# Optimization experiments

Measured on AMD Instinct MI355X. Metric: run time of the kernel, lower is better.

The kernel has to match this reference:

```python
import jax, jax.numpy as jnp
import numpy as np

B, T, N, H = 256, 128, 512, 128  # batch, timesteps, input_size (driving series), hidden


def setup_inputs() -> dict:
    key = jax.random.key(0)
    ks = jax.random.split(key, 7)
    p = lambda k, shape: (jax.random.normal(k, shape, dtype=jnp.float32) * 0.05)
    return {
        "X": jax.random.normal(ks[0], (B, T, N), dtype=jnp.float32),
        # attention linear: in_features = 2H + T, out_features = 1 (stored as a vector + scalar bias)
        "attn_w": p(ks[1], (2 * H + T,)),
        "attn_b": p(ks[2], ()),
        # LSTM cell params, PyTorch layout/gate order (i, f, g, o)
        "w_ih": p(ks[3], (4 * H, N)),
        "w_hh": p(ks[4], (4 * H, H)),
        "b_ih": p(ks[5], (4 * H,)),
        "b_hh": p(ks[6], (4 * H,)),
    }


def reference(X, attn_w, attn_b, w_ih, w_hh, b_ih, b_hh):
    Bn, Tn, Nn = X.shape
    Hh = w_hh.shape[1]
    # split the single attention weight row into the h / s / X-row pieces of the concat
    w_h, w_s, w_x = attn_w[:Hh], attn_w[Hh:2 * Hh], attn_w[2 * Hh:]
    Xp = jnp.swapaxes(X, 1, 2)            # [B, N, T]  (X.permute(0,2,1))
    x_score = Xp @ w_x                    # [B, N], time-invariant part of attention logits

    def step(carry, x_t):                 # x_t: [B, N] = X[:, t, :]
        h, c = carry
        # logits[b,i] = w_h.h[b] + w_s.c[b] + w_x.Xp[b,i] + b  (== Linear on the concat)
        score = x_score + (h @ w_h + c @ w_s + attn_b)[:, None]   # [B, N]
        alpha = jax.nn.softmax(score, axis=1)
        x_tilde = alpha * x_t                                      # [B, N]
        gates = x_tilde @ w_ih.T + h @ w_hh.T + b_ih + b_hh        # [B, 4H]
        i, f, g, o = jnp.split(gates, 4, axis=1)
        c_new = jax.nn.sigmoid(f) * c + jax.nn.sigmoid(i) * jnp.tanh(g)
        h_new = jax.nn.sigmoid(o) * jnp.tanh(c_new)
        return (h_new, c_new), (x_tilde, h_new)

    h0 = jnp.zeros((Bn, Hh), X.dtype)
    (_, _), (Xt, Xe) = jax.lax.scan(step, (h0, h0), jnp.swapaxes(X, 0, 1))
    # scan stacks along time -> [T, B, .]; return [B, T, .]
    return jnp.swapaxes(Xt, 0, 1), jnp.swapaxes(Xe, 0, 1)
```

## Files before the change

kernel.cpp:

```cpp
#include <hip/hip_runtime.h>
#include <hip/hip_bf16.h>

#define Bb 256
#define Tt 128
#define Nn 512
#define Hh 128

typedef __attribute__((ext_vector_type(4))) float floatx4;
typedef __attribute__((ext_vector_type(8))) short short8;
typedef _Float16 h2v_t __attribute__((ext_vector_type(2)));

__device__ __forceinline__ unsigned short f2bf(float f) {
  unsigned u = __float_as_uint(f);
  u += 0x7fffu + ((u >> 16) & 1u);
  return (unsigned short)(u >> 16);
}

__device__ __forceinline__ float sigmoid_fast(float x) {
  return __builtin_amdgcn_rcpf(1.f + __expf(-x));
}
__device__ __forceinline__ float tanh_fast(float x) {
  float e = __expf(2.f * x);
  return 1.f - 2.f * __builtin_amdgcn_rcpf(e + 1.f);
}

__device__ __forceinline__ void lds_barrier() {
  asm volatile("s_waitcnt lgkmcnt(0)" ::: "memory");
  __builtin_amdgcn_s_barrier();
  asm volatile("" ::: "memory");
}

__device__ __forceinline__ void async_load16(const void* g, void* lds) {
  __builtin_amdgcn_global_load_lds(
      (const __attribute__((address_space(1))) unsigned int*)g,
      (__attribute__((address_space(3))) unsigned int*)lds, 16, 0, 0);
}

#if __has_builtin(__builtin_amdgcn_fdot2)
#define FDOT2(a, b, c) __builtin_amdgcn_fdot2((a), (b), (c), false)
#else
__device__ __forceinline__ float fdot2_sw(h2v_t a, h2v_t b, float c) {
  return fmaf((float)a.x, (float)b.x, fmaf((float)a.y, (float)b.y, (c)));
}
#define FDOT2(a, b, c) fdot2_sw((a), (b), (c))
#endif

#define ROT1 0x121
#define ROT4 0x124
template <int CTRL>
__device__ __forceinline__ int rot_i(int x) {
#if __has_builtin(__builtin_amdgcn_update_dpp)
  return __builtin_amdgcn_update_dpp(0, x, CTRL, 0xf, 0xf, true);
#else
  return __shfl(x, (threadIdx.x & ~15) + (((threadIdx.x & 15) + (CTRL & 15)) & 15), 64);
#endif
}
template <int CTRL>
__device__ __forceinline__ float rot_f(float x) {
  return __uint_as_float((unsigned)rot_i<CTRL>((int)__float_as_uint(x)));
}

__global__ void prep_kernel(const float* __restrict__ w_ih,
                            const float* __restrict__ b_ih,
                            const float* __restrict__ b_hh,
                            unsigned short* __restrict__ wb,
                            float* __restrict__ bias) {
  int i = blockIdx.x * 256 + threadIdx.x;
  if (i < 4 * Hh * Nn) wb[i] = f2bf(w_ih[i]);
  if (i < 4 * Hh) bias[i] = b_ih[i] + b_hh[i];
}

__global__ __launch_bounds__(512) void alpha_kernel(const float* __restrict__ X,
                                                    const float* __restrict__ attn_w,
                                                    float* __restrict__ alpha) {
  int b = blockIdx.x;
  int tid = threadIdx.x;
  int c = tid & 127;
  int tp = tid >> 7;
  const float4* Xb = (const float4*)(X + (size_t)b * Tt * Nn) + c;
  const float* wx = attn_w + 2 * Hh;

  float4 acc = {0.f, 0.f, 0.f, 0.f};
#pragma unroll 8
  for (int tt = 0; tt < 32; ++tt) {
    int t = tp * 32 + tt;
    float4 x = Xb[(size_t)t * 128];
    float w = wx[t];
    acc.x = fmaf(x.x, w, acc.x);
    acc.y = fmaf(x.y, w, acc.y);
    acc.z = fmaf(x.z, w, acc.z);
    acc.w = fmaf(x.w, w, acc.w);
  }

  __shared__ float4 s4[512];
  __shared__ float sred[128];
  s4[tid] = acc;
  __syncthreads();

  float4 sc = {0.f, 0.f, 0.f, 0.f};
  if (tid < 128) {
    float4 a = s4[tid], b2 = s4[tid + 128], c2 = s4[tid + 256], d = s4[tid + 384];
    sc.x = a.x + b2.x + c2.x + d.x;
    sc.y = a.y + b2.y + c2.y + d.y;
    sc.z = a.z + b2.z + c2.z + d.z;
    sc.w = a.w + b2.w + c2.w + d.w;
    sred[tid] = fmaxf(fmaxf(sc.x, sc.y), fmaxf(sc.z, sc.w));
  }
  __syncthreads();
  for (int s = 64; s > 0; s >>= 1) {
    if (tid < s) sred[tid] = fmaxf(sred[tid], sred[tid + s]);
    __syncthreads();
  }
  float m = sred[0];
  __syncthreads();

  float4 e4 = {0.f, 0.f, 0.f, 0.f};
  if (tid < 128) {
    e4.x = __expf(sc.x - m);
    e4.y = __expf(sc.y - m);
    e4.z = __expf(sc.z - m);
    e4.w = __expf(sc.w - m);
    sred[tid] = e4.x + e4.y + e4.z + e4.w;
  }
  __syncthreads();
  for (int s = 64; s > 0; s >>= 1) {
    if (tid < s) sred[tid] += sred[tid + s];
    __syncthreads();
  }
  float inv = 1.f / sred[0];
  if (tid < 128) {
    float4 out;
    out.x = e4.x * inv; out.y = e4.y * inv; out.z = e4.z * inv; out.w = e4.w * inv;
    ((float4*)(alpha + (size_t)b * Nn))[tid] = out;
  }
}

__global__ __launch_bounds__(256) void scale_kernel(const float* __restrict__ X,
                                                    const float* __restrict__ alpha,
                                                    float* __restrict__ Xt,
                                                    unsigned short* __restrict__ xtb) {
  size_t i = (size_t)blockIdx.x * 256 + threadIdx.x;
  size_t e = i * 4;
  int n = (int)(e & (Nn - 1));
  int brow = (int)(e >> 9);
  int b = brow >> 7;
  float4 x = ((const float4*)X)[i];
  float4 a = *(const float4*)(alpha + (size_t)b * Nn + n);
  float4 y;
  y.x = x.x * a.x; y.y = x.y * a.y; y.z = x.z * a.z; y.w = x.w * a.w;
  ((float4*)Xt)[i] = y;
  ushort4 u;
  u.x = f2bf(y.x); u.y = f2bf(y.y); u.z = f2bf(y.z); u.w = f2bf(y.w);
  ((ushort4*)xtb)[i] = u;
}

#define GBK 64

__global__ __launch_bounds__(256) void gemm_bt(const unsigned short* __restrict__ A,
                                               const unsigned short* __restrict__ Bw,
                                               const float* __restrict__ bias,
                                               float* __restrict__ C) {
  __shared__ __align__(16) unsigned short As[128 * 64];
  __shared__ __align__(16) unsigned short Bs[128 * 64];
  const int K = 512, NO = 512;
  int tid = threadIdx.x;
  int lane = tid & 63;
  int wave = tid >> 6;
  int wm = wave & 1, wn = wave >> 1;
  int l15 = lane & 15;
  int quad = lane >> 4;
  int mtile = blockIdx.x, ntile = blockIdx.y;

  floatx4 acc[4][4];
#pragma unroll
  for (int i = 0; i < 4; ++i)
#pragma unroll
    for (int j = 0; j < 4; ++j) acc[i][j] = (floatx4){0.f, 0.f, 0.f, 0.f};

  int lr = lane >> 3;
  int lc = (lane & 7) ^ lr;
  const size_t lane_goff = (size_t)lr * K + lc * 8;
  const size_t abase = (size_t)mtile * 128 * K + lane_goff;
  const size_t bbase = (size_t)ntile * 128 * K + lane_goff;
  int sw = (quad ^ (l15 & 7)) * 8;

  for (int kb = 0; kb < K; kb += GBK) {
#pragma unroll
    for (int slot = 0; slot < 4; ++slot) {
      int r0 = slot * 32 + wave * 8;
      async_load16(A + abase + (size_t)r0 * K + kb, &As[r0 * 64]);
      async_load16(Bw + bbase + (size_t)r0 * K + kb, &Bs[r0 * 64]);
    }
    __syncthreads();
#pragma unroll
    for (int kh = 0; kh < 2; ++kh) {
      int sc = sw ^ (kh * 32);
      short8 af[4], bf[4];
#pragma unroll
      for (int i = 0; i < 4; ++i)
        af[i] = *(const short8*)(&As[(wm * 64 + i * 16 + l15) * 64 + sc]);
#pragma unroll
      for (int j = 0; j < 4; ++j)
        bf[j] = *(const short8*)(&Bs[(wn * 64 + j * 16 + l15) * 64 + sc]);
#pragma unroll
      for (int i = 0; i < 4; ++i)
#pragma unroll
        for (int j = 0; j < 4; ++j)
          acc[i][j] = __builtin_amdgcn_mfma_f32_16x16x32_bf16(af[i], bf[j], acc[i][j], 0, 0, 0);
    }
    __syncthreads();
  }

  int m0 = mtile * 128 + wm * 64;
  int n0 = ntile * 128 + wn * 64;
#pragma unroll
  for (int j = 0; j < 4; ++j) {
    int col = n0 + j * 16 + l15;
    float bsum = bias[col];
#pragma unroll
    for (int i = 0; i < 4; ++i) {
      int row = m0 + i * 16 + quad * 4;
#pragma unroll
      for (int r = 0; r < 4; ++r)
        C[(size_t)(row + r) * NO + col] = acc[i][j][r] + bsum;
    }
  }
}

__global__ __launch_bounds__(512, 1) void lstm_kernel(const float* __restrict__ G,
                                                      const float* __restrict__ w_hh,
                                                      float* __restrict__ Xe) {
  int b = blockIdx.x;
  int tid = threadIdx.x;
  int w = tid >> 6;
  int l = tid & 63;
  int ring = l >> 4;
  int r = l & 15;
  int f = r >> 2;
  int usub = r & 3;
  int ubase = w * 16 + ring * 4;
  int unit = ubase + usub;

  h2v_t wreg[64];
  {
    int idx = r;
#pragma unroll
    for (int p = 0; p < 16; ++p) {
      int j = idx;
      const float* wr = w_hh + (size_t)((j >> 2) * 128 + ubase + (j & 3)) * 128 + r * 8;
      float4 v0 = *(const float4*)(wr);
      float4 v1 = *(const float4*)(wr + 4);
      wreg[p * 4 + 0] = (h2v_t){(_Float16)v0.x, (_Float16)v0.y};
      wreg[p * 4 + 1] = (h2v_t){(_Float16)v0.z, (_Float16)v0.w};
      wreg[p * 4 + 2] = (h2v_t){(_Float16)v1.x, (_Float16)v1.y};
      wreg[p * 4 + 3] = (h2v_t){(_Float16)v1.z, (_Float16)v1.w};
      if (p < 15) idx = rot_i<ROT1>(idx);
    }
  }

  int g1 = rot_i<ROT4>(f);
  bool plus = (g1 == ((f + 1) & 3));

  __shared__ __align__(16) unsigned short h2[2][128];
  if (tid < 128) h2[0][tid] = 0;
  __syncthreads();

  const float* Gb = G + (size_t)b * Tt * 512 + f * 128 + unit;
  float* Xeb = Xe + (size_t)b * Tt * Hh;

  float gcur = Gb[0];
  float gnext = Gb[512];
  float c0 = 0.f;

  const float actm = (f == 2) ? 2.f : -1.f;
  const float fA   = (f == 2) ? -2.f : 1.f;
  const float fB   = (f == 2) ? 1.f : 0.f;

#define H2F(W) __builtin_bit_cast(h2v_t, (W))

  for (int t = 0; t < Tt; ++t) {
    int cur = t & 1;
    uint4 hq = *(const uint4*)(&h2[cur][r * 8]);

    float g_this = gcur;
    gcur = gnext;
    if (t + 2 < Tt) gnext = Gb[(size_t)(t + 2) * 512];

    float a0 = g_this, a1 = 0.f;
#pragma unroll
    for (int p = 0; p < 16; ++p) {
      a0 = FDOT2(H2F(hq.x), wreg[p * 4 + 0], a0);
      a0 = FDOT2(H2F(hq.y), wreg[p * 4 + 1], a0);
      a1 = FDOT2(H2F(hq.z), wreg[p * 4 + 2], a1);
      a1 = FDOT2(H2F(hq.w), wreg[p * 4 + 3], a1);
      a0 = rot_f<ROT1>(a0);
      a1 = rot_f<ROT1>(a1);
    }
    float x = a0 + a1;

    float e = __expf(x * actm);
    float val = fmaf(__builtin_amdgcn_rcpf(1.f + e), fA, fB);

    float x1 = rot_f<ROT4>(val);
    float x2 = rot_f<ROT4>(x1);
    float x3 = rot_f<ROT4>(x2);
    float gfv = plus ? x1 : x3;
    float gov = plus ? x3 : x1;

    if (f == 0) {
      c0 = fmaf(gfv, c0, val * x2);
      float hv = gov * tanh_fast(c0);
      h2[cur ^ 1][unit] = __builtin_bit_cast(unsigned short, (_Float16)hv);
      Xeb[(size_t)t * Hh + unit] = hv;
    }
    lds_barrier();
  }
#undef H2F
}

extern "C" void kernel_launch(void* const* d_in, const int* in_sizes, int n_in,
                              void* d_out, int out_size, void* d_ws, size_t ws_size,
                              hipStream_t stream) {
  const float* X      = (const float*)d_in[0];
  const float* attn_w = (const float*)d_in[1];
  const float* w_ih   = (const float*)d_in[3];
  const float* w_hh   = (const float*)d_in[4];
  const float* b_ih   = (const float*)d_in[5];
  const float* b_hh   = (const float*)d_in[6];

  float* Xt = (float*)d_out;
  float* Xe = (float*)d_out + (size_t)Bb * Tt * Nn;

  char* ws = (char*)d_ws;
  float*          alpha = (float*)(ws);
  float*          bias  = (float*)(ws + 524288);
  unsigned short* wb    = (unsigned short*)(ws + 526336);
  unsigned short* xtb   = (unsigned short*)(ws + 1050624);
  float*          G     = (float*)(ws + 34605056);

  prep_kernel<<<dim3(1024), dim3(256), 0, stream>>>(w_ih, b_ih, b_hh, wb, bias);
  alpha_kernel<<<dim3(Bb), dim3(512), 0, stream>>>(X, attn_w, alpha);
  scale_kernel<<<dim3(16384), dim3(256), 0, stream>>>(X, alpha, Xt, xtb);
  gemm_bt<<<dim3(256, 4), dim3(256), 0, stream>>>(xtb, wb, bias, G);
  lstm_kernel<<<dim3(Bb), dim3(512), 0, stream>>>(G, w_hh, Xe);
}
```

Before: 276.9 us.

## Restructure LSTM recurrence to 8 lanes per unit with DPP butterfly reduction

The recurrent LSTM kernel now runs 1024 threads per block, with 8 lanes per hidden unit each holding a 16-element slice of all four gate rows. Each lane does 32 fdot2 operations and the partials are combined with a three-step DPP rotate-add reduction, replacing the previous 16-step serial rotate chain through a ring of lanes. One lane per unit then applies the activations and updates the cell state. This shortens the serial dependency chain on each timestep, at the cost of more threads per block and redundant activation math being removed from the other lanes.

Measured after the change: 323.8 us. +16.9%, slower.

```diff
diff --git a/kernel.cpp b/kernel.cpp
--- a/kernel.cpp
+++ b/kernel.cpp
@@ -46,6 +46,7 @@
 #endif
 
 #define ROT1 0x121
+#define ROT2 0x122
 #define ROT4 0x124
 template <int CTRL>
 __device__ __forceinline__ int rot_i(int x) {
@@ -227,91 +228,87 @@
   }
 }
 
-__global__ __launch_bounds__(512, 1) void lstm_kernel(const float* __restrict__ G,
-                                                      const float* __restrict__ w_hh,
-                                                      float* __restrict__ Xe) {
+__global__ __launch_bounds__(1024, 1) void lstm_kernel(const float* __restrict__ G,
+                                                       const float* __restrict__ w_hh,
+                                                       float* __restrict__ Xe) {
   int b = blockIdx.x;
   int tid = threadIdx.x;
-  int w = tid >> 6;
-  int l = tid & 63;
-  int ring = l >> 4;
-  int r = l & 15;
-  int f = r >> 2;
-  int usub = r & 3;
-  int ubase = w * 16 + ring * 4;
-  int unit = ubase + usub;
-
-  h2v_t wreg[64];
-  {
-    int idx = r;
-#pragma unroll
-    for (int p = 0; p < 16; ++p) {
-      int j = idx;
-      const float* wr = w_hh + (size_t)((j >> 2) * 128 + ubase + (j & 3)) * 128 + r * 8;
-      float4 v0 = *(const float4*)(wr);
-      float4 v1 = *(const float4*)(wr + 4);
-      wreg[p * 4 + 0] = (h2v_t){(_Float16)v0.x, (_Float16)v0.y};
-      wreg[p * 4 + 1] = (h2v_t){(_Float16)v0.z, (_Float16)v0.w};
-      wreg[p * 4 + 2] = (h2v_t){(_Float16)v1.x, (_Float16)v1.y};
-      wreg[p * 4 + 3] = (h2v_t){(_Float16)v1.z, (_Float16)v1.w};
-      if (p < 15) idx = rot_i<ROT1>(idx);
-    }
-  }
-
-  int g1 = rot_i<ROT4>(f);
-  bool plus = (g1 == ((f + 1) & 3));
+  int u = tid >> 3;
+  int e = tid & 7;
+  int l15 = tid & 15;
+
+  h2v_t wreg[4][8];
+#pragma unroll
+  for (int f = 0; f < 4; ++f) {
+    const float* wr = w_hh + (size_t)(f * 128 + u) * 128 + e * 16;
+#pragma unroll
+    for (int i = 0; i < 4; ++i) {
+      float4 v = *(const float4*)(wr + i * 4);
+      wreg[f][2 * i]     = (h2v_t){(_Float16)v.x, (_Float16)v.y};
+      wreg[f][2 * i + 1] = (h2v_t){(_Float16)v.z, (_Float16)v.w};
+    }
+  }
+
+  int d1 = rot_i<ROT1>(l15);
+  bool plus = (d1 == ((l15 + 1) & 15));
+  bool amdone = (e == (plus ? 0 : 7));
+
+  float sel0 = (e == 0) ? 1.f : 0.f;
+  float sel1 = (e == 1) ? 1.f : 0.f;
+  float sel2 = (e == 2) ? 1.f : 0.f;
+  float sel3 = (e == 3) ? 1.f : 0.f;
 
   __shared__ __align__(16) unsigned short h2[2][128];
   if (tid < 128) h2[0][tid] = 0;
   __syncthreads();
 
-  const float* Gb = G + (size_t)b * Tt * 512 + f * 128 + unit;
+  const float* Gb = G + (size_t)b * Tt * 512 + (e & 3) * 128 + u;
   float* Xeb = Xe + (size_t)b * Tt * Hh;
 
   float gcur = Gb[0];
   float gnext = Gb[512];
   float c0 = 0.f;
 
-  const float actm = (f == 2) ? 2.f : -1.f;
-  const float fA   = (f == 2) ? -2.f : 1.f;
-  const float fB   = (f == 2) ? 1.f : 0.f;
-
 #define H2F(W) __builtin_bit_cast(h2v_t, (W))
 
   for (int t = 0; t < Tt; ++t) {
     int cur = t & 1;
-    uint4 hq = *(const uint4*)(&h2[cur][r * 8]);
+    const uint4* hp = (const uint4*)(&h2[cur][e * 16]);
+    uint4 ha = hp[0], hb = hp[1];
 
     float g_this = gcur;
     gcur = gnext;
     if (t + 2 < Tt) gnext = Gb[(size_t)(t + 2) * 512];
 
-    float a0 = g_this, a1 = 0.f;
-#pragma unroll
-    for (int p = 0; p < 16; ++p) {
-      a0 = FDOT2(H2F(hq.x), wreg[p * 4 + 0], a0);
-      a0 = FDOT2(H2F(hq.y), wreg[p * 4 + 1], a0);
-      a1 = FDOT2(H2F(hq.z), wreg[p * 4 + 2], a1);
-      a1 = FDOT2(H2F(hq.w), wreg[p * 4 + 3], a1);
-      a0 = rot_f<ROT1>(a0);
-      a1 = rot_f<ROT1>(a1);
-    }
-    float x = a0 + a1;
-
-    float e = __expf(x * actm);
-    float val = fmaf(__builtin_amdgcn_rcpf(1.f + e), fA, fB);
-
-    float x1 = rot_f<ROT4>(val);
-    float x2 = rot_f<ROT4>(x1);
-    float x3 = rot_f<ROT4>(x2);
-    float gfv = plus ? x1 : x3;
-    float gov = plus ? x3 : x1;
-
-    if (f == 0) {
-      c0 = fmaf(gfv, c0, val * x2);
-      float hv = gov * tanh_fast(c0);
-      h2[cur ^ 1][unit] = __builtin_bit_cast(unsigned short, (_Float16)hv);
-      Xeb[(size_t)t * Hh + unit] = hv;
+    float a0 = g_this * sel0;
+    float a1 = g_this * sel1;
+    float a2 = g_this * sel2;
+    float a3 = g_this * sel3;
+#define DK(HB, K)                                   \
+    a0 = FDOT2(H2F(HB), wreg[0][K], a0);            \
+    a1 = FDOT2(H2F(HB), wreg[1][K], a1);            \
+    a2 = FDOT2(H2F(HB), wreg[2][K], a2);            \
+    a3 = FDOT2(H2F(HB), wreg[3][K], a3);
+    DK(ha.x, 0) DK(ha.y, 1) DK(ha.z, 2) DK(ha.w, 3)
+    DK(hb.x, 4) DK(hb.y, 5) DK(hb.z, 6) DK(hb.w, 7)
+#undef DK
+
+    a0 += rot_f<ROT1>(a0); a1 += rot_f<ROT1>(a1);
+    a2 += rot_f<ROT1>(a2); a3 += rot_f<ROT1>(a3);
+    a0 += rot_f<ROT2>(a0); a1 += rot_f<ROT2>(a1);
+    a2 += rot_f<ROT2>(a2); a3 += rot_f<ROT2>(a3);
+    a0 += rot_f<ROT4>(a0); a1 += rot_f<ROT4>(a1);
+    a2 += rot_f<ROT4>(a2); a3 += rot_f<ROT4>(a3);
+
+    if (amdone) {
+      float si = sigmoid_fast(a0);
+      float sf = sigmoid_fast(a1);
+      float tg = tanh_fast(a2);
+      float so = sigmoid_fast(a3);
+      c0 = fmaf(sf, c0, si * tg);
+      float hv = so * tanh_fast(c0);
+      h2[cur ^ 1][u] = __builtin_bit_cast(unsigned short, (_Float16)hv);
+      Xeb[(size_t)t * Hh + u] = hv;
     }
     lds_barrier();
   }
@@ -342,5 +339,5 @@
   alpha_kernel<<<dim3(Bb), dim3(512), 0, stream>>>(X, attn_w, alpha);
   scale_kernel<<<dim3(16384), dim3(256), 0, stream>>>(X, alpha, Xt, xtb);
   gemm_bt<<<dim3(256, 4), dim3(256), 0, stream>>>(xtb, wb, bias, G);
-  lstm_kernel<<<dim3(Bb), dim3(512), 0, stream>>>(G, w_hh, Xe);
-}
+  lstm_kernel<<<dim3(Bb), dim3(1024), 0, stream>>>(G, w_hh, Xe);
+}
```
